# Optimization experiments

Measured on AMD Instinct MI355X. Metric: run time of the kernel, lower is better.

Reference implementation:

```python
import jax, jax.numpy as jnp
import numpy as np

N_NODES = 100000
N_EDGES = 3200000
IN_DIM, BIG, HID = 4, 32, 2
EPS = 1e-5


def _lin_init(key, fan_in, fan_out):
    # torch nn.Linear default: U(-1/sqrt(fan_in), 1/sqrt(fan_in))
    kw, kb = jax.random.split(key)
    bound = 1.0 / np.sqrt(fan_in)
    w = jax.random.uniform(kw, (fan_in, fan_out), minval=-bound, maxval=bound, dtype=jnp.float32)
    b = jax.random.uniform(kb, (fan_out,), minval=-bound, maxval=bound, dtype=jnp.float32)
    return w, b


def setup_inputs() -> dict:
    key = jax.random.key(0)
    ks = jax.random.split(key, 9)
    x = jax.random.normal(ks[0], (N_NODES, IN_DIM), dtype=jnp.float32)
    edge_index = jax.random.randint(ks[1], (2, N_EDGES), 0, N_NODES, dtype=jnp.int32)
    bn_w = jnp.ones((IN_DIM,), jnp.float32)
    bn_b = jnp.zeros((IN_DIM,), jnp.float32)
    enc_w1, enc_b1 = _lin_init(ks[2], 2 * IN_DIM, BIG)
    enc_w2, enc_b2 = _lin_init(ks[3], BIG, BIG)
    enc_w3, enc_b3 = _lin_init(ks[4], BIG, HID)
    dec_w1, dec_b1 = _lin_init(ks[5], 2 * HID, BIG)
    dec_w2, dec_b2 = _lin_init(ks[6], BIG, BIG)
    dec_w3, dec_b3 = _lin_init(ks[7], BIG, IN_DIM)
    return dict(x=x, edge_index=edge_index, bn_w=bn_w, bn_b=bn_b,
                enc_w1=enc_w1, enc_b1=enc_b1, enc_w2=enc_w2, enc_b2=enc_b2,
                enc_w3=enc_w3, enc_b3=enc_b3,
                dec_w1=dec_w1, dec_b1=dec_b1, dec_w2=dec_w2, dec_b2=dec_b2,
                dec_w3=dec_w3, dec_b3=dec_b3)


def _edge_conv(x, src, dst, w1, b1, w2, b2, w3, b3, final_relu):
    # PyG EdgeConv: message = nn(cat([x_i, x_j - x_i])), mean-aggregated at target i (=dst)
    xi = x[dst]                     # [E, F] gather (target)
    xj = x[src]                     # [E, F] gather (source)
    h = jnp.concatenate([xi, xj - xi], axis=-1)  # [E, 2F]
    h = jax.nn.relu(h @ w1 + b1)
    h = jax.nn.relu(h @ w2 + b2)
    h = h @ w3 + b3
    if final_relu:
        h = jax.nn.relu(h)
    n = x.shape[0]
    agg = jax.ops.segment_sum(h, dst, num_segments=n)          # [N, out]
    cnt = jax.ops.segment_sum(jnp.ones((h.shape[0],), h.dtype), dst, num_segments=n)
    return agg / jnp.maximum(cnt, 1.0)[:, None]


def reference(x, edge_index, bn_w, bn_b,
              enc_w1, enc_b1, enc_w2, enc_b2, enc_w3, enc_b3,
              dec_w1, dec_b1, dec_w2, dec_b2, dec_w3, dec_b3):
    # BatchNorm1d (training mode: batch statistics, biased variance)
    mu = jnp.mean(x, axis=0)
    var = jnp.var(x, axis=0)
    h = (x - mu) * jax.lax.rsqrt(var + EPS) * bn_w + bn_b
    src, dst = edge_index[0], edge_index[1]
    h = _edge_conv(h, src, dst, enc_w1, enc_b1, enc_w2, enc_b2, enc_w3, enc_b3, final_relu=True)
    h = _edge_conv(h, src, dst, dec_w1, dec_b1, dec_w2, dec_b2, dec_w3, dec_b3, final_relu=False)
    return h
```

## Files before the change

### kernel.cpp

```cpp
#include <hip/hip_runtime.h>

#define N_NODES 100000
#define N_EDGES 3200000
#define EPS 1e-5f
#define NODE_BLOCKS 391
#define NB 782
#define BSTRIDE 4608
#define NSUB 3
#define S1_EPB 4096
#define S1_BLOCKS 782

typedef unsigned int uint;
typedef uint u32x4 __attribute__((ext_vector_type(4)));
typedef _Float16 f16x8 __attribute__((ext_vector_type(8)));
typedef float f32x16 __attribute__((ext_vector_type(16)));

static __device__ __forceinline__ f16x8 as_h8(u32x4 u) { return __builtin_bit_cast(f16x8, u); }
static __device__ __forceinline__ uint pkh(float a, float b) {
    return __builtin_bit_cast(uint, __builtin_amdgcn_cvt_pkrtz(a, b));
}
static __device__ __forceinline__ void swap32(uint& a, uint& b) {
    asm volatile("v_permlane32_swap_b32 %0, %1" : "+v"(a), "+v"(b));
}
static __device__ __forceinline__ uint prelu(uint u, uint z) {
    uint r;
    asm("v_pk_max_f16 %0, %1, %2" : "=v"(r) : "v"(u), "v"(z));
    return r;
}

#define MFMA(A, B, C) __builtin_amdgcn_mfma_f32_32x32x16_f16(as_h8(A), as_h8(B), (C), 0, 0, 0)

static __device__ __forceinline__ void repack(const f32x16& c, u32x4& f0, u32x4& f1, uint z) {
    uint p0 = prelu(pkh(c[0], c[1]), z),   p1 = prelu(pkh(c[2], c[3]), z);
    uint q0 = prelu(pkh(c[4], c[5]), z),   q1 = prelu(pkh(c[6], c[7]), z);
    uint p2 = prelu(pkh(c[8], c[9]), z),   p3 = prelu(pkh(c[10], c[11]), z);
    uint q2 = prelu(pkh(c[12], c[13]), z), q3 = prelu(pkh(c[14], c[15]), z);
    swap32(p0, q0); swap32(p1, q1);
    swap32(p2, q2); swap32(p3, q3);
    f0.x = p0; f0.y = p1; f0.z = q0; f0.w = q1;
    f1.x = p2; f1.y = p3; f1.z = q2; f1.w = q3;
}

static __device__ __forceinline__ void decode4(const int4& q, int* ss, int* ia) {
    int e0 = q.x, e1 = q.y, e2 = q.z, e3 = q.w;
    ss[0] = e0 & 0x1FFFF; ia[0] = (e0 >> 17) & 127;
    ss[1] = e1 & 0x1FFFF; ia[1] = (e1 >> 17) & 127;
    ss[2] = e2 & 0x1FFFF; ia[2] = (e2 >> 17) & 127;
    ss[3] = e3 & 0x1FFFF; ia[3] = (e3 >> 17) & 127;
    #pragma unroll
    for (int k = 0; k < 4; k++)
        if (ss[k] >= N_NODES) ss[k] = 0;
}

#define OFF_STATS  0
#define OFF_BCNT   1024
#define OFF_INVCNT 5120
#define OFF_AGG1   405120
#define OFF_DECW   1205120
#define OFF_BUCKET 1214848
#define OFF_PENC   15629696
#define OFF_PCNT   22836608
#define OFF_PDEC   26440064
#define OFF_ENCW   26440064


__global__ __launch_bounds__(256) void k_bn_stats(const float* __restrict__ x,
                                                  double* __restrict__ stats) {
    int i = blockIdx.x * 256 + threadIdx.x;
    float4 v = make_float4(0.f, 0.f, 0.f, 0.f);
    if (i < N_NODES) v = ((const float4*)x)[i];
    double a[8];
    a[0] = v.x; a[1] = v.y; a[2] = v.z; a[3] = v.w;
    a[4] = (double)v.x * v.x; a[5] = (double)v.y * v.y;
    a[6] = (double)v.z * v.z; a[7] = (double)v.w * v.w;
    #pragma unroll
    for (int off = 32; off > 0; off >>= 1) {
        #pragma unroll
        for (int j = 0; j < 8; j++) a[j] += __shfl_down(a[j], off);
    }
    __shared__ double smem[4][8];
    int wave = threadIdx.x >> 6;
    int lane = threadIdx.x & 63;
    if (lane == 0) {
        #pragma unroll
        for (int j = 0; j < 8; j++) smem[wave][j] = a[j];
    }
    __syncthreads();
    if (threadIdx.x == 0) {
        #pragma unroll
        for (int j = 0; j < 8; j++) {
            double t = smem[0][j] + smem[1][j] + smem[2][j] + smem[3][j];
            atomicAdd(&stats[j], t);
        }
    }
}

static __device__ __forceinline__ uint pk_part(float a, float b, int part) {
    _Float16 ah = (_Float16)a, bh = (_Float16)b;
    if (part) {
        a -= (float)ah; b -= (float)bh;
        ah = (_Float16)a; bh = (_Float16)b;
    }
    return (uint)__builtin_bit_cast(unsigned short, ah) |
           ((uint)__builtin_bit_cast(unsigned short, bh) << 16);
}

__global__ __launch_bounds__(256) void k_prep(const double* __restrict__ stats,
                                              const float* __restrict__ bn_w,
                                              const float* __restrict__ bn_b,
                                              const float* __restrict__ ew1,
                                              const float* __restrict__ eb1,
                                              const float* __restrict__ ew2,
                                              const float* __restrict__ eb2,
                                              const float* __restrict__ ew3,
                                              const float* __restrict__ eb3,
                                              const float* __restrict__ dw1,
                                              const float* __restrict__ db1,
                                              const float* __restrict__ dw2,
                                              const float* __restrict__ db2,
                                              const float* __restrict__ dw3,
                                              const float* __restrict__ db3,
                                              uint* __restrict__ encw,
                                              uint* __restrict__ decw) {
    int t = threadIdx.x;
    int lane = t >> 2, d = t & 3;
    int hi = lane >> 5, m = lane & 31;

    const double inv_n = 1.0 / (double)N_NODES;
    float sc[4], sh[4];
    #pragma unroll
    for (int dd = 0; dd < 4; dd++) {
        double mu = stats[dd] * inv_n;
        double vr = stats[4 + dd] * inv_n - mu * mu;
        float rs = (float)(1.0 / sqrt(vr + (double)EPS));
        sc[dd] = rs * bn_w[dd];
        sh[dd] = bn_b[dd] - (float)mu * sc[dd];
    }
    float b1p = eb1[m];
    #pragma unroll
    for (int dd = 0; dd < 4; dd++) b1p += ew1[dd * 32 + m] * sh[dd];

    int k0 = 8 * hi + 2 * d;
    {
        float v0 = (k0 < 8) ? ew1[k0 * 32 + m] * sc[k0 & 3]
                            : (k0 == 8 ? b1p : 0.f);
        float v1 = (k0 + 1 < 8) ? ew1[(k0 + 1) * 32 + m] * sc[(k0 + 1) & 3] : 0.f;
        encw[t] = pk_part(v0, v1, 0);
        encw[256 + t] = pk_part(v0, v1, 1);
    }
    {
        float v0 = (k0 < 4) ? dw1[k0 * 32 + m] : (k0 == 4 ? db1[m] : 0.f);
        float v1 = (k0 + 1 < 4) ? dw1[(k0 + 1) * 32 + m] : 0.f;
        decw[t] = pk_part(v0, v1, 0);
        decw[256 + t] = pk_part(v0, v1, 1);
    }
    #pragma unroll
    for (int tile = 0; tile < 2; tile++) {
        int k = 16 * tile + k0;
        {
            float a = ew2[k * 32 + m], bb = ew2[(k + 1) * 32 + m];
            encw[512 + tile * 256 + t] = pk_part(a, bb, 0);
            encw[1024 + tile * 256 + t] = pk_part(a, bb, 1);
        }
        {
            float a = dw2[k * 32 + m], bb = dw2[(k + 1) * 32 + m];
            decw[512 + tile * 256 + t] = pk_part(a, bb, 0);
            decw[1024 + tile * 256 + t] = pk_part(a, bb, 1);
        }
        {
            float a = 0.f, bb = 0.f;
            if (m == 0 || m == 4) {
                int o = m >> 2;
                a = ew3[k * 2 + o]; bb = ew3[(k + 1) * 2 + o];
            }
            encw[1536 + tile * 256 + t] = pk_part(a, bb, 0);
        }
        {
            float a = 0.f, bb = 0.f;
            if ((m & 3) < 2 && m < 6) {
                int o = (m & 1) + 2 * (m >> 2);
                a = dw3[k * 4 + o]; bb = dw3[(k + 1) * 4 + o];
            }
            decw[1536 + tile * 256 + t] = pk_part(a, bb, 0);
        }
    }
    if (t < 32) {
        int hh = t >> 4, r = t & 15;
        int row = (r & 3) + 8 * (r >> 2) + 4 * hh;
        ((float*)encw)[2048 + t] = eb2[row];
        ((float*)encw)[2080 + t] = (row == 0) ? eb3[0] : (row == 4) ? eb3[1] : 0.f;
        ((float*)decw)[2048 + t] = db2[row];
        ((float*)decw)[2080 + t] =
            ((row & 3) < 2 && row < 6) ? db3[(row & 1) + 2 * (row >> 2)] : 0.f;
    }
}

__global__ __launch_bounds__(256) void k_s1(const int* __restrict__ ei,
                                            int* __restrict__ bcnt,
                                            int* __restrict__ bucket_buf) {
    __shared__ int hist[NB];
    __shared__ int base[NB];
    __shared__ int run[NB];
    __shared__ int gbase[NB];
    __shared__ int entries[S1_EPB];
    __shared__ unsigned short bk16[S1_EPB];
    __shared__ int wsum[4];
    int tid = threadIdx.x;
    int e0 = blockIdx.x * S1_EPB;
    for (int i = tid; i < NB; i += 256) hist[i] = 0;
    __syncthreads();
    #pragma unroll
    for (int k = 0; k < S1_EPB / 256; k++) {
        int e = e0 + k * 256 + tid;
        if (e < N_EDGES) atomicAdd(&hist[ei[N_EDGES + e] >> 7], 1);
    }
    __syncthreads();
    int t4 = tid * 4;
    int h0 = (t4 + 0 < NB) ? hist[t4 + 0] : 0;
    int h1 = (t4 + 1 < NB) ? hist[t4 + 1] : 0;
    int h2 = (t4 + 2 < NB) ? hist[t4 + 2] : 0;
    int h3 = (t4 + 3 < NB) ? hist[t4 + 3] : 0;
    int tsum = h0 + h1 + h2 + h3;
    int lane = tid & 63, wv = tid >> 6;
    int xs = tsum;
    #pragma unroll
    for (int off = 1; off < 64; off <<= 1) {
        int u = __shfl_up(xs, off);
        if (lane >= off) xs += u;
    }
    if (lane == 63) wsum[wv] = xs;
    __syncthreads();
    int wo = 0;
    #pragma unroll
    for (int w = 0; w < 4; w++) if (w < wv) wo += wsum[w];
    int texcl = wo + xs - tsum;
    if (t4 + 0 < NB) base[t4 + 0] = texcl;
    if (t4 + 1 < NB) base[t4 + 1] = texcl + h0;
    if (t4 + 2 < NB) base[t4 + 2] = texcl + h0 + h1;
    if (t4 + 3 < NB) base[t4 + 3] = texcl + h0 + h1 + h2;
    __syncthreads();
    for (int i = tid; i < NB; i += 256) {
        int h = hist[i];
        gbase[i] = i * BSTRIDE + (h ? atomicAdd(&bcnt[i], h) : 0);
        run[i] = base[i];
    }
    __syncthreads();
    #pragma unroll
    for (int k = 0; k < S1_EPB / 256; k++) {
        int e = e0 + k * 256 + tid;
        if (e < N_EDGES) {
            int s = ei[e];
            int d = ei[N_EDGES + e];
            int b = d >> 7;
            int r = atomicAdd(&run[b], 1);
            entries[r] = s | ((d & 127) << 17);
            bk16[r] = (unsigned short)b;
        }
    }
    __syncthreads();
    int nloc = min(S1_EPB, N_EDGES - e0);
    for (int idx = tid; idx < nloc; idx += 256) {
        int b = bk16[idx];
        bucket_buf[gbase[b] + (idx - base[b])] = entries[idx];
    }
}

__global__ __launch_bounds__(256, 4) void k_enc_partial(const float* __restrict__ x,
                                                        const int* __restrict__ bucket_buf,
                                                        const int* __restrict__ bcnt,
                                                        float2* __restrict__ penc,
                                                        int* __restrict__ pcnt,
                                                        const uint* __restrict__ encw) {
    __shared__ float4 xs[128];
    __shared__ float acc0[128], acc1[128];
    __shared__ int lc[128];
    int b = blockIdx.x, sub = blockIdx.y, tid = threadIdx.x;
    int lane = tid & 63, hi = lane >> 5, col = lane & 31, wv = tid >> 6;
    int cb = bcnt[b];
    int node0 = b << 7;

    if (tid < 128) {
        acc0[tid] = 0.f; acc1[tid] = 0.f; lc[tid] = 0;
        int n = node0 + tid;
        if (n >= N_NODES) n = 0;
        xs[tid] = ((const float4*)x)[n];
    }
    __syncthreads();

    const u32x4* W4 = (const u32x4*)encw;
    u32x4 w1h  = W4[lane],       w1l  = W4[64 + lane];
    u32x4 w2h0 = W4[128 + lane], w2h1 = W4[192 + lane];
    u32x4 w2l0 = W4[256 + lane], w2l1 = W4[320 + lane];
    u32x4 w30  = W4[384 + lane], w31  = W4[448 + lane];
    const float* tf = (const float*)encw;
    f32x16 b2f;
    {
        const float4* p2 = (const float4*)(tf + 2048 + hi * 16);
        #pragma unroll
        for (int q = 0; q < 4; q++) {
            float4 c = p2[q];
            b2f[4 * q] = c.x; b2f[4 * q + 1] = c.y; b2f[4 * q + 2] = c.z; b2f[4 * q + 3] = c.w;
        }
    }
    float bc0 = tf[2080 + hi * 16] - b2f[0];
    float* accH = hi ? acc1 : acc0;
    uint z = 0;

    int wb0 = sub * 1536 + wv * 128;
    if (wb0 < cb) {
        const int4* BB = (const int4*)&bucket_buf[b * BSTRIDE];
        int i0 = (wb0 >> 2) + col;
        int4 qa = BB[i0];
        int4 qb = BB[i0 + 128];
        int4 qc = BB[i0 + 256];
        bool act1 = (wb0 + 512) < cb;
        bool act2 = (wb0 + 1024) < cb;

        auto enc_win = [&](const int* ia, const float4* xg, int wb) {
            #pragma unroll
            for (int j = 0; j < 4; j++) {
                u32x4 xf;
                if (hi == 0) {
                    float4 xi = xs[ia[j]];
                    xf.x = pkh(xi.x, xi.y);
                    xf.y = pkh(xi.z, xi.w);
                    xf.z = pkh(xg[j].x - xi.x, xg[j].y - xi.y);
                    xf.w = pkh(xg[j].z - xi.z, xg[j].w - xi.w);
                } else {
                    xf.x = 0x00003C00u;
                    xf.y = 0u; xf.z = 0u; xf.w = 0u;
                }
                f32x16 c = {};
                c = MFMA(w1h, xf, c);
                c = MFMA(w1l, xf, c);
                u32x4 f0, f1;
                repack(c, f0, f1, z);
                f32x16 c2 = MFMA(w2h0, f0, b2f);
                c2 = MFMA(w2h1, f1, c2);
                c2 = MFMA(w2l0, f0, c2);
                c2 = MFMA(w2l1, f1, c2);
                u32x4 e0, e1;
                repack(c2, e0, e1, z);
                f32x16 c3 = MFMA(w30, e0, b2f);
                c3 = MFMA(w31, e1, c3);
                float o = fmaxf(c3[0] + bc0, 0.f);
                if ((wb + col * 4 + j) < cb) {
                    atomicAdd(&accH[ia[j]], o);
                    if (hi == 0) atomicAdd(&lc[ia[j]], 1);
                }
            }
        };

        int s0[4], s1[4], s2[4], ia0[4], ia1[4], ia2[4];
        float4 xg0[4], xg1[4], xg2[4];
        decode4(qa, s0, ia0);
        if (hi == 0) {
            #pragma unroll
            for (int k = 0; k < 4; k++) xg0[k] = ((const float4*)x)[s0[k]];
        }
        if (act1) {
            decode4(qb, s1, ia1);
            if (hi == 0) {
                #pragma unroll
                for (int k = 0; k < 4; k++) xg1[k] = ((const float4*)x)[s1[k]];
            }
        }
        enc_win(ia0, xg0, wb0);
        if (act2) {
            decode4(qc, s2, ia2);
            if (hi == 0) {
                #pragma unroll
                for (int k = 0; k < 4; k++) xg2[k] = ((const float4*)x)[s2[k]];
            }
        }
        if (act1) enc_win(ia1, xg1, wb0 + 512);
        if (act2) enc_win(ia2, xg2, wb0 + 1024);
    }
    __syncthreads();
    if (tid < 128) {
        int pb = b * NSUB + sub;
        penc[pb * 128 + tid] = make_float2(acc0[tid], acc1[tid]);
        pcnt[pb * 128 + tid] = lc[tid];
    }
}

__global__ __launch_bounds__(256) void k_reduce_enc_p(const float2* __restrict__ penc,
                                                      const int* __restrict__ pcnt,
                                                      float2* __restrict__ agg1,
                                                      float* __restrict__ invcnt) {
    int i = blockIdx.x * 256 + threadIdx.x;
    if (i >= N_NODES) return;
    int b = i >> 7, l = i & 127;
    float a0 = 0.f, a1 = 0.f;
    int c = 0;
    #pragma unroll
    for (int sub = 0; sub < NSUB; sub++) {
        int idx = (b * NSUB + sub) * 128 + l;
        float2 p = penc[idx];
        a0 += p.x; a1 += p.y;
        c += pcnt[idx];
    }
    float ic = 1.0f / (float)(c > 1 ? c : 1);
    invcnt[i] = ic;
    agg1[i] = make_float2(a0 * ic, a1 * ic);
}

__global__ __launch_bounds__(256, 4) void k_dec_partial(const float2* __restrict__ henc,
                                                        const int* __restrict__ bucket_buf,
                                                        const int* __restrict__ bcnt,
                                                        float4* __restrict__ pdec,
                                                        const uint* __restrict__ decw) {
    __shared__ float2 hld[128];
    __shared__ float a0s[128], a1s[128], a2s[128], a3s[128];
    int b = blockIdx.x, sub = blockIdx.y, tid = threadIdx.x;
    int lane = tid & 63, hi = lane >> 5, col = lane & 31, wv = tid >> 6;
    int cb = bcnt[b];
    int node0 = b << 7;

    if (tid < 128) {
        a0s[tid] = 0.f; a1s[tid] = 0.f; a2s[tid] = 0.f; a3s[tid] = 0.f;
        int n = node0 + tid;
        if (n >= N_NODES) n = 0;
        hld[tid] = henc[n];
    }
    __syncthreads();

    const u32x4* W4 = (const u32x4*)decw;
    u32x4 w1h  = W4[lane],       w1l  = W4[64 + lane];
    u32x4 v2h0 = W4[128 + lane], v2h1 = W4[192 + lane];
    u32x4 v2l0 = W4[256 + lane], v2l1 = W4[320 + lane];
    u32x4 w30  = W4[384 + lane], w31  = W4[448 + lane];
    const float* tf = (const float*)decw;
    f32x16 b2f;
    {
        const float4* p2 = (const float4*)(tf + 2048 + hi * 16);
        #pragma unroll
        for (int q = 0; q < 4; q++) {
            float4 c = p2[q];
            b2f[4 * q] = c.x; b2f[4 * q + 1] = c.y; b2f[4 * q + 2] = c.z; b2f[4 * q + 3] = c.w;
        }
    }
    float bc0 = tf[2080 + hi * 16 + 0] - b2f[0];
    float bc1 = tf[2080 + hi * 16 + 1] - b2f[1];
    float* accA = hi ? a2s : a0s;
    float* accB = hi ? a3s : a1s;
    uint z = 0;

    int wb0 = sub * 1536 + wv * 128;
    if (wb0 < cb) {
        const int4* BB = (const int4*)&bucket_buf[b * BSTRIDE];
        int i0 = (wb0 >> 2) + col;
        int4 qa = BB[i0];
        int4 qb = BB[i0 + 128];
        int4 qc = BB[i0 + 256];
        bool act1 = (wb0 + 512) < cb;
        bool act2 = (wb0 + 1024) < cb;

        auto dec_win = [&](const int* ia, const float2* hj, int wb) {
            #pragma unroll
            for (int j = 0; j < 4; j++) {
                u32x4 xf;
                if (hi == 0) {
                    float2 h2 = hld[ia[j]];
                    xf.x = pkh(h2.x, h2.y);
                    xf.y = pkh(hj[j].x - h2.x, hj[j].y - h2.y);
                    xf.z = 0x00003C00u;
                    xf.w = 0u;
                } else {
                    xf.x = 0u; xf.y = 0u; xf.z = 0u; xf.w = 0u;
                }
                f32x16 c = {};
                c = MFMA(w1h, xf, c);
                c = MFMA(w1l, xf, c);
                u32x4 f0, f1;
                repack(c, f0, f1, z);
                f32x16 c2 = MFMA(v2h0, f0, b2f);
                c2 = MFMA(v2h1, f1, c2);
                c2 = MFMA(v2l0, f0, c2);
                c2 = MFMA(v2l1, f1, c2);
                u32x4 e0, e1;
                repack(c2, e0, e1, z);
                f32x16 c3 = MFMA(w30, e0, b2f);
                c3 = MFMA(w31, e1, c3);
                float o0 = c3[0] + bc0;
                float o1 = c3[1] + bc1;
                if ((wb + col * 4 + j) < cb) {
                    atomicAdd(&accA[ia[j]], o0);
                    atomicAdd(&accB[ia[j]], o1);
                }
            }
        };

        int s0[4], s1[4], s2[4], ia0[4], ia1[4], ia2[4];
        float2 hg0[4], hg1[4], hg2[4];
        decode4(qa, s0, ia0);
        if (hi == 0) {
            #pragma unroll
            for (int k = 0; k < 4; k++) hg0[k] = henc[s0[k]];
        }
        if (act1) {
            decode4(qb, s1, ia1);
            if (hi == 0) {
                #pragma unroll
                for (int k = 0; k < 4; k++) hg1[k] = henc[s1[k]];
            }
        }
        dec_win(ia0, hg0, wb0);
        if (act2) {
            decode4(qc, s2, ia2);
            if (hi == 0) {
                #pragma unroll
                for (int k = 0; k < 4; k++) hg2[k] = henc[s2[k]];
            }
        }
        if (act1) dec_win(ia1, hg1, wb0 + 512);
        if (act2) dec_win(ia2, hg2, wb0 + 1024);
    }
    __syncthreads();
    if (tid < 128) {
        int pb = b * NSUB + sub;
        pdec[pb * 128 + tid] = make_float4(a0s[tid], a1s[tid], a2s[tid], a3s[tid]);
    }
}

__global__ __launch_bounds__(256) void k_reduce_dec_p(const float4* __restrict__ pdec,
                                                      const float* __restrict__ invcnt,
                                                      float4* __restrict__ out) {
    int i = blockIdx.x * 256 + threadIdx.x;
    if (i >= N_NODES) return;
    int b = i >> 7, l = i & 127;
    float a0 = 0.f, a1 = 0.f, a2 = 0.f, a3 = 0.f;
    #pragma unroll
    for (int sub = 0; sub < NSUB; sub++) {
        float4 p = pdec[(b * NSUB + sub) * 128 + l];
        a0 += p.x; a1 += p.y; a2 += p.z; a3 += p.w;
    }
    float ic = invcnt[i];
    out[i] = make_float4(a0 * ic, a1 * ic, a2 * ic, a3 * ic);
}

extern "C" void kernel_launch(void* const* d_in, const int* in_sizes, int n_in,
                              void* d_out, int out_size, void* d_ws, size_t ws_size,
                              hipStream_t stream) {
    const float* x    = (const float*)d_in[0];
    const int*   ei   = (const int*)d_in[1];
    const float* bn_w = (const float*)d_in[2];
    const float* bn_b = (const float*)d_in[3];
    const float* ew1  = (const float*)d_in[4];
    const float* eb1  = (const float*)d_in[5];
    const float* ew2  = (const float*)d_in[6];
    const float* eb2  = (const float*)d_in[7];
    const float* ew3  = (const float*)d_in[8];
    const float* eb3  = (const float*)d_in[9];
    const float* dw1  = (const float*)d_in[10];
    const float* db1  = (const float*)d_in[11];
    const float* dw2  = (const float*)d_in[12];
    const float* db2  = (const float*)d_in[13];
    const float* dw3  = (const float*)d_in[14];
    const float* db3  = (const float*)d_in[15];

    char* ws = (char*)d_ws;
    double* stats      = (double*)(ws + OFF_STATS);
    int*    bcnt       = (int*)(ws + OFF_BCNT);
    float*  invcnt     = (float*)(ws + OFF_INVCNT);
    float2* agg1       = (float2*)(ws + OFF_AGG1);
    uint*   decw       = (uint*)(ws + OFF_DECW);
    int*    bucket_buf = (int*)(ws + OFF_BUCKET);
    float2* penc       = (float2*)(ws + OFF_PENC);
    int*    pcnt       = (int*)(ws + OFF_PCNT);
    float4* pdec       = (float4*)(ws + OFF_PDEC);
    uint*   encw       = (uint*)(ws + OFF_ENCW);
    float4* out        = (float4*)d_out;

    hipMemsetAsync(ws, 0, 5120, stream);

    k_bn_stats<<<NODE_BLOCKS, 256, 0, stream>>>(x, stats);
    k_prep<<<1, 256, 0, stream>>>(stats, bn_w, bn_b, ew1, eb1, ew2, eb2, ew3, eb3,
                                  dw1, db1, dw2, db2, dw3, db3, encw, decw);
    k_s1<<<S1_BLOCKS, 256, 0, stream>>>(ei, bcnt, bucket_buf);
    k_enc_partial<<<dim3(NB, NSUB), 256, 0, stream>>>(x, bucket_buf, bcnt,
                                                      penc, pcnt, encw);
    k_reduce_enc_p<<<NODE_BLOCKS, 256, 0, stream>>>(penc, pcnt, agg1, invcnt);
    k_dec_partial<<<dim3(NB, NSUB), 256, 0, stream>>>(agg1, bucket_buf, bcnt, pdec, decw);
    k_reduce_dec_p<<<NODE_BLOCKS, 256, 0, stream>>>(pdec, invcnt, out);
}
```

Measured before the change: 310.9 us.

## Fuse partial reductions into single-block-per-bucket edge kernels and merge BN stats

Removes the three-way sub-split of each destination bucket, so one block now walks every edge of its bucket in a software-pipelined loop that prefetches the next window's indices and gathers. The block writes the normalized result directly, which eliminates both partial buffers and both separate reduce kernels. BatchNorm statistics are folded into the bucketing kernel, whose blocks now cover twice as many edges each. This cuts two to three launches and the partial-buffer traffic, but drops grid size from 2346 to 782 blocks, which lowers parallelism and exposes load imbalance across buckets.

```diff
diff --git a/kernel.cpp b/kernel.cpp
--- a/kernel.cpp
+++ b/kernel.cpp
@@ -3,12 +3,10 @@
 #define N_NODES 100000
 #define N_EDGES 3200000
 #define EPS 1e-5f
-#define NODE_BLOCKS 391
 #define NB 782
 #define BSTRIDE 4608
-#define NSUB 3
-#define S1_EPB 4096
-#define S1_BLOCKS 782
+#define S1_EPB 8192
+#define S1_BLOCKS 391
 
 typedef unsigned int uint;
 typedef uint u32x4 __attribute__((ext_vector_type(4)));
@@ -41,59 +39,14 @@
     f1.x = p2; f1.y = p3; f1.z = q2; f1.w = q3;
 }
 
-static __device__ __forceinline__ void decode4(const int4& q, int* ss, int* ia) {
-    int e0 = q.x, e1 = q.y, e2 = q.z, e3 = q.w;
-    ss[0] = e0 & 0x1FFFF; ia[0] = (e0 >> 17) & 127;
-    ss[1] = e1 & 0x1FFFF; ia[1] = (e1 >> 17) & 127;
-    ss[2] = e2 & 0x1FFFF; ia[2] = (e2 >> 17) & 127;
-    ss[3] = e3 & 0x1FFFF; ia[3] = (e3 >> 17) & 127;
-    #pragma unroll
-    for (int k = 0; k < 4; k++)
-        if (ss[k] >= N_NODES) ss[k] = 0;
-}
-
 #define OFF_STATS  0
 #define OFF_BCNT   1024
 #define OFF_INVCNT 5120
 #define OFF_AGG1   405120
 #define OFF_DECW   1205120
 #define OFF_BUCKET 1214848
-#define OFF_PENC   15629696
-#define OFF_PCNT   22836608
-#define OFF_PDEC   26440064
-#define OFF_ENCW   26440064
-
-
-__global__ __launch_bounds__(256) void k_bn_stats(const float* __restrict__ x,
-                                                  double* __restrict__ stats) {
-    int i = blockIdx.x * 256 + threadIdx.x;
-    float4 v = make_float4(0.f, 0.f, 0.f, 0.f);
-    if (i < N_NODES) v = ((const float4*)x)[i];
-    double a[8];
-    a[0] = v.x; a[1] = v.y; a[2] = v.z; a[3] = v.w;
-    a[4] = (double)v.x * v.x; a[5] = (double)v.y * v.y;
-    a[6] = (double)v.z * v.z; a[7] = (double)v.w * v.w;
-    #pragma unroll
-    for (int off = 32; off > 0; off >>= 1) {
-        #pragma unroll
-        for (int j = 0; j < 8; j++) a[j] += __shfl_down(a[j], off);
-    }
-    __shared__ double smem[4][8];
-    int wave = threadIdx.x >> 6;
-    int lane = threadIdx.x & 63;
-    if (lane == 0) {
-        #pragma unroll
-        for (int j = 0; j < 8; j++) smem[wave][j] = a[j];
-    }
-    __syncthreads();
-    if (threadIdx.x == 0) {
-        #pragma unroll
-        for (int j = 0; j < 8; j++) {
-            double t = smem[0][j] + smem[1][j] + smem[2][j] + smem[3][j];
-            atomicAdd(&stats[j], t);
-        }
-    }
-}
+#define OFF_ENCW   15629696
+
 
 static __device__ __forceinline__ uint pk_part(float a, float b, int part) {
     _Float16 ah = (_Float16)a, bh = (_Float16)b;
@@ -195,7 +148,9 @@
     }
 }
 
-__global__ __launch_bounds__(256) void k_s1(const int* __restrict__ ei,
+__global__ __launch_bounds__(256) void k_s1(const float* __restrict__ x,
+                                            double* __restrict__ stats,
+                                            const int* __restrict__ ei,
                                             int* __restrict__ bcnt,
                                             int* __restrict__ bucket_buf) {
     __shared__ int hist[NB];
@@ -205,7 +160,37 @@
     __shared__ int entries[S1_EPB];
     __shared__ unsigned short bk16[S1_EPB];
     __shared__ int wsum[4];
+    __shared__ double smem_bn[4][8];
     int tid = threadIdx.x;
+
+    {
+        int i = blockIdx.x * 256 + tid;
+        float4 v = make_float4(0.f, 0.f, 0.f, 0.f);
+        if (i < N_NODES) v = ((const float4*)x)[i];
+        double a[8];
+        a[0] = v.x; a[1] = v.y; a[2] = v.z; a[3] = v.w;
+        a[4] = (double)v.x * v.x; a[5] = (double)v.y * v.y;
+        a[6] = (double)v.z * v.z; a[7] = (double)v.w * v.w;
+        #pragma unroll
+        for (int off = 32; off > 0; off >>= 1) {
+            #pragma unroll
+            for (int j = 0; j < 8; j++) a[j] += __shfl_down(a[j], off);
+        }
+        int wave = tid >> 6, lane = tid & 63;
+        if (lane == 0) {
+            #pragma unroll
+            for (int j = 0; j < 8; j++) smem_bn[wave][j] = a[j];
+        }
+        __syncthreads();
+        if (tid == 0) {
+            #pragma unroll
+            for (int j = 0; j < 8; j++) {
+                double t2 = smem_bn[0][j] + smem_bn[1][j] + smem_bn[2][j] + smem_bn[3][j];
+                atomicAdd(&stats[j], t2);
+            }
+        }
+    }
+
     int e0 = blockIdx.x * S1_EPB;
     for (int i = tid; i < NB; i += 256) hist[i] = 0;
     __syncthreads();
@@ -268,13 +253,13 @@
 __global__ __launch_bounds__(256, 4) void k_enc_partial(const float* __restrict__ x,
                                                         const int* __restrict__ bucket_buf,
                                                         const int* __restrict__ bcnt,
-                                                        float2* __restrict__ penc,
-                                                        int* __restrict__ pcnt,
+                                                        float2* __restrict__ agg1,
+                                                        float* __restrict__ invcnt,
                                                         const uint* __restrict__ encw) {
     __shared__ float4 xs[128];
     __shared__ float acc0[128], acc1[128];
     __shared__ int lc[128];
-    int b = blockIdx.x, sub = blockIdx.y, tid = threadIdx.x;
+    int b = blockIdx.x, tid = threadIdx.x;
     int lane = tid & 63, hi = lane >> 5, col = lane & 31, wv = tid >> 6;
     int cb = bcnt[b];
     int node0 = b << 7;
@@ -302,117 +287,120 @@
             b2f[4 * q] = c.x; b2f[4 * q + 1] = c.y; b2f[4 * q + 2] = c.z; b2f[4 * q + 3] = c.w;
         }
     }
-    float bc0 = tf[2080 + hi * 16] - b2f[0];
+    float bc0 = tf[2048 + 32 + hi * 16] - b2f[0];
     float* accH = hi ? acc1 : acc0;
     uint z = 0;
 
-    int wb0 = sub * 1536 + wv * 128;
-    if (wb0 < cb) {
+    auto tile = [&](int ian, const float4& g, int slot) {
+        u32x4 xf;
+        if (hi == 0) {
+            float4 xi = xs[ian];
+            xf.x = pkh(xi.x, xi.y);
+            xf.y = pkh(xi.z, xi.w);
+            xf.z = pkh(g.x - xi.x, g.y - xi.y);
+            xf.w = pkh(g.z - xi.z, g.w - xi.w);
+        } else {
+            xf.x = 0x00003C00u;
+            xf.y = 0u; xf.z = 0u; xf.w = 0u;
+        }
+        f32x16 c = {};
+        c = MFMA(w1h, xf, c);
+        c = MFMA(w1l, xf, c);
+        u32x4 f0, f1;
+        repack(c, f0, f1, z);
+        f32x16 c2 = MFMA(w2h0, f0, b2f);
+        c2 = MFMA(w2h1, f1, c2);
+        c2 = MFMA(w2l0, f0, c2);
+        c2 = MFMA(w2l1, f1, c2);
+        u32x4 e0, e1;
+        repack(c2, e0, e1, z);
+        f32x16 c3 = MFMA(w30, e0, b2f);
+        c3 = MFMA(w31, e1, c3);
+        float o = fmaxf(c3[0] + bc0, 0.f);
+        if (slot < cb) {
+            atomicAdd(&accH[ian], o);
+            if (hi == 0) atomicAdd(&lc[ian], 1);
+        }
+    };
+
+    int wb = wv * 128;
+    if (wb < cb) {
         const int4* BB = (const int4*)&bucket_buf[b * BSTRIDE];
-        int i0 = (wb0 >> 2) + col;
-        int4 qa = BB[i0];
-        int4 qb = BB[i0 + 128];
-        int4 qc = BB[i0 + 256];
-        bool act1 = (wb0 + 512) < cb;
-        bool act2 = (wb0 + 1024) < cb;
-
-        auto enc_win = [&](const int* ia, const float4* xg, int wb) {
-            #pragma unroll
-            for (int j = 0; j < 4; j++) {
-                u32x4 xf;
+        int i0 = wv * 32 + col;
+        int iaA, iaB, iaC, iaD;
+        float4 gA, gB, gC, gD;
+        {
+            int4 q = BB[i0];
+            int s0 = q.x & 0x1FFFF, s1 = q.y & 0x1FFFF;
+            int s2 = q.z & 0x1FFFF, s3 = q.w & 0x1FFFF;
+            if (s0 >= N_NODES) s0 = 0;
+            if (s1 >= N_NODES) s1 = 0;
+            if (s2 >= N_NODES) s2 = 0;
+            if (s3 >= N_NODES) s3 = 0;
+            iaA = (q.x >> 17) & 127; iaB = (q.y >> 17) & 127;
+            iaC = (q.z >> 17) & 127; iaD = (q.w >> 17) & 127;
+            if (hi == 0) {
+                gA = ((const float4*)x)[s0];
+                gB = ((const float4*)x)[s1];
+                gC = ((const float4*)x)[s2];
+                gD = ((const float4*)x)[s3];
+            }
+        }
+        #pragma unroll 1
+        for (int w = 0; ; w++) {
+            int wbn = wb + 512;
+            bool more = wbn < cb;
+            int nA = 0, nB = 0, nC = 0, nD = 0;
+            float4 hA, hB, hC, hD;
+            if (more) {
+                int4 q = BB[i0 + (w + 1) * 128];
+                int s0 = q.x & 0x1FFFF, s1 = q.y & 0x1FFFF;
+                int s2 = q.z & 0x1FFFF, s3 = q.w & 0x1FFFF;
+                if (s0 >= N_NODES) s0 = 0;
+                if (s1 >= N_NODES) s1 = 0;
+                if (s2 >= N_NODES) s2 = 0;
+                if (s3 >= N_NODES) s3 = 0;
+                nA = (q.x >> 17) & 127; nB = (q.y >> 17) & 127;
+                nC = (q.z >> 17) & 127; nD = (q.w >> 17) & 127;
                 if (hi == 0) {
-                    float4 xi = xs[ia[j]];
-                    xf.x = pkh(xi.x, xi.y);
-                    xf.y = pkh(xi.z, xi.w);
-                    xf.z = pkh(xg[j].x - xi.x, xg[j].y - xi.y);
-                    xf.w = pkh(xg[j].z - xi.z, xg[j].w - xi.w);
-                } else {
-                    xf.x = 0x00003C00u;
-                    xf.y = 0u; xf.z = 0u; xf.w = 0u;
+                    hA = ((const float4*)x)[s0];
+                    hB = ((const float4*)x)[s1];
+                    hC = ((const float4*)x)[s2];
+                    hD = ((const float4*)x)[s3];
                 }
-                f32x16 c = {};
-                c = MFMA(w1h, xf, c);
-                c = MFMA(w1l, xf, c);
-                u32x4 f0, f1;
-                repack(c, f0, f1, z);
-                f32x16 c2 = MFMA(w2h0, f0, b2f);
-                c2 = MFMA(w2h1, f1, c2);
-                c2 = MFMA(w2l0, f0, c2);
-                c2 = MFMA(w2l1, f1, c2);
-                u32x4 e0, e1;
-                repack(c2, e0, e1, z);
-                f32x16 c3 = MFMA(w30, e0, b2f);
-                c3 = MFMA(w31, e1, c3);
-                float o = fmaxf(c3[0] + bc0, 0.f);
-                if ((wb + col * 4 + j) < cb) {
-                    atomicAdd(&accH[ia[j]], o);
-                    if (hi == 0) atomicAdd(&lc[ia[j]], 1);
-                }
-            }
-        };
-
-        int s0[4], s1[4], s2[4], ia0[4], ia1[4], ia2[4];
-        float4 xg0[4], xg1[4], xg2[4];
-        decode4(qa, s0, ia0);
-        if (hi == 0) {
-            #pragma unroll
-            for (int k = 0; k < 4; k++) xg0[k] = ((const float4*)x)[s0[k]];
-        }
-        if (act1) {
-            decode4(qb, s1, ia1);
-            if (hi == 0) {
-                #pragma unroll
-                for (int k = 0; k < 4; k++) xg1[k] = ((const float4*)x)[s1[k]];
-            }
-        }
-        enc_win(ia0, xg0, wb0);
-        if (act2) {
-            decode4(qc, s2, ia2);
-            if (hi == 0) {
-                #pragma unroll
-                for (int k = 0; k < 4; k++) xg2[k] = ((const float4*)x)[s2[k]];
-            }
-        }
-        if (act1) enc_win(ia1, xg1, wb0 + 512);
-        if (act2) enc_win(ia2, xg2, wb0 + 1024);
+            }
+            int sl = wb + col * 4;
+            tile(iaA, gA, sl);
+            tile(iaB, gB, sl + 1);
+            tile(iaC, gC, sl + 2);
+            tile(iaD, gD, sl + 3);
+            if (!more) break;
+            iaA = nA; iaB = nB; iaC = nC; iaD = nD;
+            gA = hA; gB = hB; gC = hC; gD = hD;
+            wb = wbn;
+        }
     }
     __syncthreads();
     if (tid < 128) {
-        int pb = b * NSUB + sub;
-        penc[pb * 128 + tid] = make_float2(acc0[tid], acc1[tid]);
-        pcnt[pb * 128 + tid] = lc[tid];
-    }
-}
-
-__global__ __launch_bounds__(256) void k_reduce_enc_p(const float2* __restrict__ penc,
-                                                      const int* __restrict__ pcnt,
-                                                      float2* __restrict__ agg1,
-                                                      float* __restrict__ invcnt) {
-    int i = blockIdx.x * 256 + threadIdx.x;
-    if (i >= N_NODES) return;
-    int b = i >> 7, l = i & 127;
-    float a0 = 0.f, a1 = 0.f;
-    int c = 0;
-    #pragma unroll
-    for (int sub = 0; sub < NSUB; sub++) {
-        int idx = (b * NSUB + sub) * 128 + l;
-        float2 p = penc[idx];
-        a0 += p.x; a1 += p.y;
-        c += pcnt[idx];
-    }
-    float ic = 1.0f / (float)(c > 1 ? c : 1);
-    invcnt[i] = ic;
-    agg1[i] = make_float2(a0 * ic, a1 * ic);
+        int n = node0 + tid;
+        if (n < N_NODES) {
+            int c = lc[tid];
+            float ic = 1.0f / (float)(c > 1 ? c : 1);
+            invcnt[n] = ic;
+            agg1[n] = make_float2(acc0[tid] * ic, acc1[tid] * ic);
+        }
+    }
 }
 
 __global__ __launch_bounds__(256, 4) void k_dec_partial(const float2* __restrict__ henc,
                                                         const int* __restrict__ bucket_buf,
                                                         const int* __restrict__ bcnt,
-                                                        float4* __restrict__ pdec,
+                                                        const float* __restrict__ invcnt,
+                                                        float4* __restrict__ out,
                                                         const uint* __restrict__ decw) {
     __shared__ float2 hld[128];
     __shared__ float a0s[128], a1s[128], a2s[128], a3s[128];
-    int b = blockIdx.x, sub = blockIdx.y, tid = threadIdx.x;
+    int b = blockIdx.x, tid = threadIdx.x;
     int lane = tid & 63, hi = lane >> 5, col = lane & 31, wv = tid >> 6;
     int cb = bcnt[b];
     int node0 = b << 7;
@@ -440,103 +428,104 @@
             b2f[4 * q] = c.x; b2f[4 * q + 1] = c.y; b2f[4 * q + 2] = c.z; b2f[4 * q + 3] = c.w;
         }
     }
-    float bc0 = tf[2080 + hi * 16 + 0] - b2f[0];
-    float bc1 = tf[2080 + hi * 16 + 1] - b2f[1];
+    float bc0 = tf[2048 + 32 + hi * 16 + 0] - b2f[0];
+    float bc1 = tf[2048 + 32 + hi * 16 + 1] - b2f[1];
     float* accA = hi ? a2s : a0s;
     float* accB = hi ? a3s : a1s;
     uint z = 0;
 
-    int wb0 = sub * 1536 + wv * 128;
-    if (wb0 < cb) {
+    auto tile = [&](int ian, const float2& g, int slot) {
+        u32x4 xf;
+        if (hi == 0) {
+            float2 h2 = hld[ian];
+            xf.x = pkh(h2.x, h2.y);
+            xf.y = pkh(g.x - h2.x, g.y - h2.y);
+            xf.z = 0x00003C00u;
+            xf.w = 0u;
+        } else {
+            xf.x = 0u; xf.y = 0u; xf.z = 0u; xf.w = 0u;
+        }
+        f32x16 c = {};
+        c = MFMA(w1h, xf, c);
+        c = MFMA(w1l, xf, c);
+        u32x4 f0, f1;
+        repack(c, f0, f1, z);
+        f32x16 c2 = MFMA(v2h0, f0, b2f);
+        c2 = MFMA(v2h1, f1, c2);
+        c2 = MFMA(v2l0, f0, c2);
+        c2 = MFMA(v2l1, f1, c2);
+        u32x4 e0, e1;
+        repack(c2, e0, e1, z);
+        f32x16 c3 = MFMA(w30, e0, b2f);
+        c3 = MFMA(w31, e1, c3);
+        float o0 = c3[0] + bc0;
+        float o1 = c3[1] + bc1;
+        if (slot < cb) {
+            atomicAdd(&accA[ian], o0);
+            atomicAdd(&accB[ian], o1);
+        }
+    };
+
+    int wb = wv * 128;
+    if (wb < cb) {
         const int4* BB = (const int4*)&bucket_buf[b * BSTRIDE];
-        int i0 = (wb0 >> 2) + col;
-        int4 qa = BB[i0];
-        int4 qb = BB[i0 + 128];
-        int4 qc = BB[i0 + 256];
-        bool act1 = (wb0 + 512) < cb;
-        bool act2 = (wb0 + 1024) < cb;
-
-        auto dec_win = [&](const int* ia, const float2* hj, int wb) {
-            #pragma unroll
-            for (int j = 0; j < 4; j++) {
-                u32x4 xf;
+        int i0 = wv * 32 + col;
+        int iaA, iaB, iaC, iaD;
+        float2 gA, gB, gC, gD;
+        {
+            int4 q = BB[i0];
+            int s0 = q.x & 0x1FFFF, s1 = q.y & 0x1FFFF;
+            int s2 = q.z & 0x1FFFF, s3 = q.w & 0x1FFFF;
+            if (s0 >= N_NODES) s0 = 0;
+            if (s1 >= N_NODES) s1 = 0;
+            if (s2 >= N_NODES) s2 = 0;
+            if (s3 >= N_NODES) s3 = 0;
+            iaA = (q.x >> 17) & 127; iaB = (q.y >> 17) & 127;
+            iaC = (q.z >> 17) & 127; iaD = (q.w >> 17) & 127;
+            if (hi == 0) {
+                gA = henc[s0]; gB = henc[s1]; gC = henc[s2]; gD = henc[s3];
+            }
+        }
+        #pragma unroll 1
+        for (int w = 0; ; w++) {
+            int wbn = wb + 512;
+            bool more = wbn < cb;
+            int nA = 0, nB = 0, nC = 0, nD = 0;
+            float2 hA, hB, hC, hD;
+            if (more) {
+                int4 q = BB[i0 + (w + 1) * 128];
+                int s0 = q.x & 0x1FFFF, s1 = q.y & 0x1FFFF;
+                int s2 = q.z & 0x1FFFF, s3 = q.w & 0x1FFFF;
+                if (s0 >= N_NODES) s0 = 0;
+                if (s1 >= N_NODES) s1 = 0;
+                if (s2 >= N_NODES) s2 = 0;
+                if (s3 >= N_NODES) s3 = 0;
+                nA = (q.x >> 17) & 127; nB = (q.y >> 17) & 127;
+                nC = (q.z >> 17) & 127; nD = (q.w >> 17) & 127;
                 if (hi == 0) {
-                    float2 h2 = hld[ia[j]];
-                    xf.x = pkh(h2.x, h2.y);
-                    xf.y = pkh(hj[j].x - h2.x, hj[j].y - h2.y);
-                    xf.z = 0x00003C00u;
-                    xf.w = 0u;
-                } else {
-                    xf.x = 0u; xf.y = 0u; xf.z = 0u; xf.w = 0u;
+                    hA = henc[s0]; hB = henc[s1]; hC = henc[s2]; hD = henc[s3];
                 }
-                f32x16 c = {};
-                c = MFMA(w1h, xf, c);
-                c = MFMA(w1l, xf, c);
-                u32x4 f0, f1;
-                repack(c, f0, f1, z);
-                f32x16 c2 = MFMA(v2h0, f0, b2f);
-                c2 = MFMA(v2h1, f1, c2);
-                c2 = MFMA(v2l0, f0, c2);
-                c2 = MFMA(v2l1, f1, c2);
-                u32x4 e0, e1;
-                repack(c2, e0, e1, z);
-                f32x16 c3 = MFMA(w30, e0, b2f);
-                c3 = MFMA(w31, e1, c3);
-                float o0 = c3[0] + bc0;
-                float o1 = c3[1] + bc1;
-                if ((wb + col * 4 + j) < cb) {
-                    atomicAdd(&accA[ia[j]], o0);
-                    atomicAdd(&accB[ia[j]], o1);
-                }
-            }
-        };
-
-        int s0[4], s1[4], s2[4], ia0[4], ia1[4], ia2[4];
-        float2 hg0[4], hg1[4], hg2[4];
-        decode4(qa, s0, ia0);
-        if (hi == 0) {
-            #pragma unroll
-            for (int k = 0; k < 4; k++) hg0[k] = henc[s0[k]];
-        }
-        if (act1) {
-            decode4(qb, s1, ia1);
-            if (hi == 0) {
-                #pragma unroll
-                for (int k = 0; k < 4; k++) hg1[k] = henc[s1[k]];
-            }
-        }
-        dec_win(ia0, hg0, wb0);
-        if (act2) {
-            decode4(qc, s2, ia2);
-            if (hi == 0) {
-                #pragma unroll
-                for (int k = 0; k < 4; k++) hg2[k] = henc[s2[k]];
-            }
-        }
-        if (act1) dec_win(ia1, hg1, wb0 + 512);
-        if (act2) dec_win(ia2, hg2, wb0 + 1024);
+            }
+            int sl = wb + col * 4;
+            tile(iaA, gA, sl);
+            tile(iaB, gB, sl + 1);
+            tile(iaC, gC, sl + 2);
+            tile(iaD, gD, sl + 3);
+            if (!more) break;
+            iaA = nA; iaB = nB; iaC = nC; iaD = nD;
+            gA = hA; gB = hB; gC = hC; gD = hD;
+            wb = wbn;
+        }
     }
     __syncthreads();
     if (tid < 128) {
-        int pb = b * NSUB + sub;
-        pdec[pb * 128 + tid] = make_float4(a0s[tid], a1s[tid], a2s[tid], a3s[tid]);
-    }
-}
-
-__global__ __launch_bounds__(256) void k_reduce_dec_p(const float4* __restrict__ pdec,
-                                                      const float* __restrict__ invcnt,
-                                                      float4* __restrict__ out) {
-    int i = blockIdx.x * 256 + threadIdx.x;
-    if (i >= N_NODES) return;
-    int b = i >> 7, l = i & 127;
-    float a0 = 0.f, a1 = 0.f, a2 = 0.f, a3 = 0.f;
-    #pragma unroll
-    for (int sub = 0; sub < NSUB; sub++) {
-        float4 p = pdec[(b * NSUB + sub) * 128 + l];
-        a0 += p.x; a1 += p.y; a2 += p.z; a3 += p.w;
-    }
-    float ic = invcnt[i];
-    out[i] = make_float4(a0 * ic, a1 * ic, a2 * ic, a3 * ic);
+        int n = node0 + tid;
+        if (n < N_NODES) {
+            float ic = invcnt[n];
+            out[n] = make_float4(a0s[tid] * ic, a1s[tid] * ic,
+                                 a2s[tid] * ic, a3s[tid] * ic);
+        }
+    }
 }
 
 extern "C" void kernel_launch(void* const* d_in, const int* in_sizes, int n_in,
@@ -566,21 +555,14 @@
     float2* agg1       = (float2*)(ws + OFF_AGG1);
     uint*   decw       = (uint*)(ws + OFF_DECW);
     int*    bucket_buf = (int*)(ws + OFF_BUCKET);
-    float2* penc       = (float2*)(ws + OFF_PENC);
-    int*    pcnt       = (int*)(ws + OFF_PCNT);
-    float4* pdec       = (float4*)(ws + OFF_PDEC);
     uint*   encw       = (uint*)(ws + OFF_ENCW);
     float4* out        = (float4*)d_out;
 
     hipMemsetAsync(ws, 0, 5120, stream);
 
-    k_bn_stats<<<NODE_BLOCKS, 256, 0, stream>>>(x, stats);
+    k_s1<<<S1_BLOCKS, 256, 0, stream>>>(x, stats, ei, bcnt, bucket_buf);
     k_prep<<<1, 256, 0, stream>>>(stats, bn_w, bn_b, ew1, eb1, ew2, eb2, ew3, eb3,
                                   dw1, db1, dw2, db2, dw3, db3, encw, decw);
-    k_s1<<<S1_BLOCKS, 256, 0, stream>>>(ei, bcnt, bucket_buf);
-    k_enc_partial<<<dim3(NB, NSUB), 256, 0, stream>>>(x, bucket_buf, bcnt,
-                                                      penc, pcnt, encw);
-    k_reduce_enc_p<<<NODE_BLOCKS, 256, 0, stream>>>(penc, pcnt, agg1, invcnt);
-    k_dec_partial<<<dim3(NB, NSUB), 256, 0, stream>>>(agg1, bucket_buf, bcnt, pdec, decw);
-    k_reduce_dec_p<<<NODE_BLOCKS, 256, 0, stream>>>(pdec, invcnt, out);
-}
+    k_enc_partial<<<NB, 256, 0, stream>>>(x, bucket_buf, bcnt, agg1, invcnt, encw);
+    k_dec_partial<<<NB, 256, 0, stream>>>(agg1, bucket_buf, bcnt, invcnt, out, decw);
+}
```

After: 310.8 us. No clear change (-0.0%).
